# Performance work log

Hardware: AMD Instinct MI355X
Metric: run time of the kernel (lower is better)

## Reference

```python
import jax, jax.numpy as jnp
import numpy as np

B = 2048   # number of sessions
L = 128    # items per session (uniform sessions)
IDCG_FLOOR = 1e-5


def _pairwise_diff(t):
    # t: [L] -> [L, L] with m[i, j] = t[i] - t[j]
    return t[:, None] - t[None, :]


def _position_discounts(t):
    # rank of each element under descending sort, then 1/log2(rank+2)
    ranks = jnp.argsort(jnp.argsort(-t))
    return 1.0 / jnp.log2(ranks.astype(jnp.float32) + 2.0)


def _per_session(pred, label):
    # defaults: use_exp_gain=True, use_ndcg_as_loss=True, use_idcg_normalization=True
    gain = jnp.exp2(label).astype(jnp.float32)
    pred_disc = _position_discounts(pred)
    label_disc = _position_discounts(label)
    idcg = jnp.maximum(gain @ label_disc, IDCG_FLOOR)
    dcg = gain @ pred_disc
    session_weight = idcg  # use_idcg_normalization=True
    sign = jnp.sign(_pairwise_diff(label))
    pd_lxp = sign * _pairwise_diff(pred)
    lambda_mat = jnp.abs(_pairwise_diff(pred_disc) * _pairwise_diff(gain))
    loss = (idcg - dcg) / session_weight  # use_ndcg_as_loss=True
    grad_loss = jnp.sum(-lambda_mat * sign * jax.nn.sigmoid(-pd_lxp), axis=1) / session_weight
    return loss, grad_loss


def setup_inputs() -> dict:
    key = jax.random.key(0)
    k1, k2 = jax.random.split(key)
    logit = jax.random.normal(k1, (B * L,), dtype=jnp.float32)
    label = jax.random.randint(k2, (B * L,), 0, 5).astype(jnp.float32)
    return {"logit": logit, "label": label}


def reference(logit, label):
    # sessions are uniform length L, grouped contiguously -> reshape to [B, L]
    loss, grad_loss = jax.vmap(_per_session)(logit.reshape(B, L), label.reshape(B, L))
    return loss, grad_loss.reshape(-1)
```

## Files before the change

kernel.cpp:

```cpp
#include <hip/hip_runtime.h>
#include <math.h>

#define NSESS 2048
#define L 128
#define IDCG_FLOOR 1e-5f
#define LOG2E 1.44269504088896340736f

__device__ __forceinline__ float rl_f(float x, int j) {
    return __uint_as_float((unsigned)__builtin_amdgcn_readlane((int)__float_as_uint(x), j));
}
__device__ __forceinline__ unsigned rl_u(unsigned x, int j) {
    return (unsigned)__builtin_amdgcn_readlane((int)x, j);
}
__device__ __forceinline__ float fast_exp2(float x) {
    float r;
    asm("v_exp_f32 %0, %1" : "=v"(r) : "v"(x));
    return r;
}

__global__ __launch_bounds__(64) void lambdarank_ndcg_kernel(
    const float* __restrict__ logit,
    const float* __restrict__ label,
    float* __restrict__ out_loss,
    float* __restrict__ out_grad)
{
    const int b    = blockIdx.x;
    const int lane = threadIdx.x;
    const int base = b * L;

    const float p0  = logit[base + lane];
    const float p1  = logit[base + 64 + lane];
    const float lb0 = label[base + lane];
    const float lb1 = label[base + 64 + lane];
    const int   il0 = (int)lb0;
    const int   il1 = (int)lb1;
    const float g0  = (float)(1 << il0);
    const float g1  = (float)(1 << il1);

    const unsigned bb0  = __float_as_uint(p0);
    const unsigned bb1  = __float_as_uint(p1);
    const unsigned asc0 = (bb0 & 0x80000000u) ? ~bb0 : (bb0 | 0x80000000u);
    const unsigned asc1 = (bb1 & 0x80000000u) ? ~bb1 : (bb1 | 0x80000000u);
    const unsigned long long K0 =
        (((unsigned long long)(~asc0)) << 7) | (unsigned)lane;
    const unsigned long long K1 =
        (((unsigned long long)(~asc1)) << 7) | (unsigned)(lane + 64);

    int rp0 = 0, rp1 = 0;
    #pragma unroll 8
    for (int j = 0; j < 64; ++j) {
        const unsigned lo = rl_u((unsigned)K0, j);
        const unsigned hi = rl_u((unsigned)(K0 >> 32), j);
        const unsigned long long Kj = (((unsigned long long)hi) << 32) | lo;
        rp0 += (Kj < K0);
        rp1 += (Kj < K1);
    }
    #pragma unroll 8
    for (int j = 0; j < 64; ++j) {
        const unsigned lo = rl_u((unsigned)K1, j);
        const unsigned hi = rl_u((unsigned)(K1 >> 32), j);
        const unsigned long long Kj = (((unsigned long long)hi) << 32) | lo;
        rp0 += (Kj < K0);
        rp1 += (Kj < K1);
    }

    const unsigned long long lane_lt = (1ull << lane) - 1ull;
    int rl0 = 0, rl1 = 0;
    {
        int sumG = 0;
        #pragma unroll
        for (int v = 4; v >= 0; --v) {
            const unsigned long long m0 = __ballot(il0 == v);
            const unsigned long long m1 = __ballot(il1 == v);
            if (il0 == v) rl0 = sumG + __popcll(m0 & lane_lt);
            if (il1 == v) rl1 = sumG + __popcll(m0) + __popcll(m1 & lane_lt);
            sumG += __popcll(m0) + __popcll(m1);
        }
    }

    const float pd0 = __builtin_amdgcn_rcpf(log2f((float)(rp0 + 2)));
    const float pd1 = __builtin_amdgcn_rcpf(log2f((float)(rp1 + 2)));
    const float ld0 = __builtin_amdgcn_rcpf(log2f((float)(rl0 + 2)));
    const float ld1 = __builtin_amdgcn_rcpf(log2f((float)(rl1 + 2)));

    float dcg  = g0 * pd0 + g1 * pd1;
    float idcg = g0 * ld0 + g1 * ld1;
    #pragma unroll
    for (int off = 32; off > 0; off >>= 1) {
        dcg  += __shfl_xor(dcg,  off, 64);
        idcg += __shfl_xor(idcg, off, 64);
    }
    const float IDCG     = fmaxf(idcg, IDCG_FLOOR);
    const float inv_idcg = __builtin_amdgcn_rcpf(IDCG);

    const float ps0 = p0 * LOG2E;
    const float ps1 = p1 * LOG2E;
    float acc0 = 0.0f, acc1 = 0.0f;

    #pragma unroll 4
    for (int j = 0; j < 64; ++j) {
        const float pj = rl_f(ps0, j);
        const float gj = rl_f(g0,  j);
        const float dj = rl_f(pd0, j);
        {
            const float e  = fast_exp2(ps0 - pj);
            const float sg = __builtin_amdgcn_rcpf(1.0f + e);
            const float t  = (pd0 - dj) * (g0 - gj);
            const float nm = ((g0 < gj) ? 1.0f : 0.0f) - sg;
            acc0 += fabsf(t) * nm;
        }
        {
            const float e  = fast_exp2(ps1 - pj);
            const float sg = __builtin_amdgcn_rcpf(1.0f + e);
            const float t  = (pd1 - dj) * (g1 - gj);
            const float nm = ((g1 < gj) ? 1.0f : 0.0f) - sg;
            acc1 += fabsf(t) * nm;
        }
    }
    #pragma unroll 4
    for (int j = 0; j < 64; ++j) {
        const float pj = rl_f(ps1, j);
        const float gj = rl_f(g1,  j);
        const float dj = rl_f(pd1, j);
        {
            const float e  = fast_exp2(ps0 - pj);
            const float sg = __builtin_amdgcn_rcpf(1.0f + e);
            const float t  = (pd0 - dj) * (g0 - gj);
            const float nm = ((g0 < gj) ? 1.0f : 0.0f) - sg;
            acc0 += fabsf(t) * nm;
        }
        {
            const float e  = fast_exp2(ps1 - pj);
            const float sg = __builtin_amdgcn_rcpf(1.0f + e);
            const float t  = (pd1 - dj) * (g1 - gj);
            const float nm = ((g1 < gj) ? 1.0f : 0.0f) - sg;
            acc1 += fabsf(t) * nm;
        }
    }

    out_grad[base + lane]      = acc0 * inv_idcg;
    out_grad[base + 64 + lane] = acc1 * inv_idcg;
    if (lane == 0) out_loss[b] = (IDCG - dcg) * inv_idcg;
}

extern "C" void kernel_launch(void* const* d_in, const int* in_sizes, int n_in,
                              void* d_out, int out_size, void* d_ws, size_t ws_size,
                              hipStream_t stream) {
    const float* logit = (const float*)d_in[0];
    const float* label = (const float*)d_in[1];
    float* out      = (float*)d_out;
    float* out_loss = out;
    float* out_grad = out + NSESS;

    lambdarank_ndcg_kernel<<<NSESS, 64, 0, stream>>>(logit, label, out_loss, out_grad);
}
```

Measured before the change: 75.33 us.

## Factor sigmoid exponent into per-element exp products and vectorize loads

The per-pair exp2(pi - pj) is replaced by the product exp2(pi)*exp2(-pj), with both factors precomputed once per element. This removes one transcendental from the inner O(L^2) loop and leaves one multiply-add and one reciprocal per pair. Each lane now owns two adjacent elements, so loads and stores become float2, and the tie-break indices and label-rank prefix counts are adjusted to the interleaved order. Log and reciprocal use raw hardware instructions, and the unroll goes from 4 to 8. The product form can overflow to inf or underflow for large logit gaps, which changes precision at the extremes.

After: 72.51 us. -3.7%, faster.

```diff
diff --git a/kernel.cpp b/kernel.cpp
--- a/kernel.cpp
+++ b/kernel.cpp
@@ -12,11 +12,9 @@
 __device__ __forceinline__ unsigned rl_u(unsigned x, int j) {
     return (unsigned)__builtin_amdgcn_readlane((int)x, j);
 }
-__device__ __forceinline__ float fast_exp2(float x) {
-    float r;
-    asm("v_exp_f32 %0, %1" : "=v"(r) : "v"(x));
-    return r;
-}
+__device__ __forceinline__ float fexp2(float x){ float r; asm("v_exp_f32 %0, %1":"=v"(r):"v"(x)); return r; }
+__device__ __forceinline__ float flog2(float x){ float r; asm("v_log_f32 %0, %1":"=v"(r):"v"(x)); return r; }
+__device__ __forceinline__ float frcp (float x){ float r; asm("v_rcp_f32 %0, %1":"=v"(r):"v"(x)); return r; }
 
 __global__ __launch_bounds__(64) void lambdarank_ndcg_kernel(
     const float* __restrict__ logit,
@@ -28,10 +26,10 @@
     const int lane = threadIdx.x;
     const int base = b * L;
 
-    const float p0  = logit[base + lane];
-    const float p1  = logit[base + 64 + lane];
-    const float lb0 = label[base + lane];
-    const float lb1 = label[base + 64 + lane];
+    const float2 pv = ((const float2*)(logit + base))[lane];
+    const float2 lv = ((const float2*)(label + base))[lane];
+    const float p0  = pv.x,  p1  = pv.y;
+    const float lb0 = lv.x,  lb1 = lv.y;
     const int   il0 = (int)lb0;
     const int   il1 = (int)lb1;
     const float g0  = (float)(1 << il0);
@@ -42,9 +40,9 @@
     const unsigned asc0 = (bb0 & 0x80000000u) ? ~bb0 : (bb0 | 0x80000000u);
     const unsigned asc1 = (bb1 & 0x80000000u) ? ~bb1 : (bb1 | 0x80000000u);
     const unsigned long long K0 =
-        (((unsigned long long)(~asc0)) << 7) | (unsigned)lane;
+        (((unsigned long long)(~asc0)) << 7) | (unsigned)(2 * lane);
     const unsigned long long K1 =
-        (((unsigned long long)(~asc1)) << 7) | (unsigned)(lane + 64);
+        (((unsigned long long)(~asc1)) << 7) | (unsigned)(2 * lane + 1);
 
     int rp0 = 0, rp1 = 0;
     #pragma unroll 8
@@ -65,6 +63,7 @@
     }
 
     const unsigned long long lane_lt = (1ull << lane) - 1ull;
+    const unsigned long long lane_le = lane_lt | (1ull << lane);
     int rl0 = 0, rl1 = 0;
     {
         int sumG = 0;
@@ -72,16 +71,16 @@
         for (int v = 4; v >= 0; --v) {
             const unsigned long long m0 = __ballot(il0 == v);
             const unsigned long long m1 = __ballot(il1 == v);
-            if (il0 == v) rl0 = sumG + __popcll(m0 & lane_lt);
-            if (il1 == v) rl1 = sumG + __popcll(m0) + __popcll(m1 & lane_lt);
+            if (il0 == v) rl0 = sumG + __popcll(m0 & lane_lt) + __popcll(m1 & lane_lt);
+            if (il1 == v) rl1 = sumG + __popcll(m0 & lane_le) + __popcll(m1 & lane_lt);
             sumG += __popcll(m0) + __popcll(m1);
         }
     }
 
-    const float pd0 = __builtin_amdgcn_rcpf(log2f((float)(rp0 + 2)));
-    const float pd1 = __builtin_amdgcn_rcpf(log2f((float)(rp1 + 2)));
-    const float ld0 = __builtin_amdgcn_rcpf(log2f((float)(rl0 + 2)));
-    const float ld1 = __builtin_amdgcn_rcpf(log2f((float)(rl1 + 2)));
+    const float pd0 = frcp(flog2((float)(rp0 + 2)));
+    const float pd1 = frcp(flog2((float)(rp1 + 2)));
+    const float ld0 = frcp(flog2((float)(rl0 + 2)));
+    const float ld1 = frcp(flog2((float)(rl1 + 2)));
 
     float dcg  = g0 * pd0 + g1 * pd1;
     float idcg = g0 * ld0 + g1 * ld1;
@@ -91,55 +90,47 @@
         idcg += __shfl_xor(idcg, off, 64);
     }
     const float IDCG     = fmaxf(idcg, IDCG_FLOOR);
-    const float inv_idcg = __builtin_amdgcn_rcpf(IDCG);
+    const float inv_idcg = frcp(IDCG);
 
-    const float ps0 = p0 * LOG2E;
-    const float ps1 = p1 * LOG2E;
+    const float ps0   = p0 * LOG2E;
+    const float ps1   = p1 * LOG2E;
+    const float E0    = fexp2(ps0);
+    const float E1    = fexp2(ps1);
+    const float Einv0 = fexp2(-ps0);
+    const float Einv1 = fexp2(-ps1);
+
     float acc0 = 0.0f, acc1 = 0.0f;
 
-    #pragma unroll 4
+    #pragma unroll 8
     for (int j = 0; j < 64; ++j) {
-        const float pj = rl_f(ps0, j);
-        const float gj = rl_f(g0,  j);
-        const float dj = rl_f(pd0, j);
-        {
-            const float e  = fast_exp2(ps0 - pj);
-            const float sg = __builtin_amdgcn_rcpf(1.0f + e);
-            const float t  = (pd0 - dj) * (g0 - gj);
-            const float nm = ((g0 < gj) ? 1.0f : 0.0f) - sg;
-            acc0 += fabsf(t) * nm;
-        }
-        {
-            const float e  = fast_exp2(ps1 - pj);
-            const float sg = __builtin_amdgcn_rcpf(1.0f + e);
-            const float t  = (pd1 - dj) * (g1 - gj);
-            const float nm = ((g1 < gj) ? 1.0f : 0.0f) - sg;
-            acc1 += fabsf(t) * nm;
-        }
+        const float EJ = rl_f(Einv0, j);
+        const float gj = rl_f(g0,   j);
+        const float dj = rl_f(pd0,  j);
+        const float sg0 = frcp(1.0f + E0 * EJ);
+        const float sg1 = frcp(1.0f + E1 * EJ);
+        const float t0  = (pd0 - dj) * (g0 - gj);
+        const float t1  = (pd1 - dj) * (g1 - gj);
+        const float nm0 = ((g0 < gj) ? 1.0f : 0.0f) - sg0;
+        const float nm1 = ((g1 < gj) ? 1.0f : 0.0f) - sg1;
+        acc0 = fmaf(fabsf(t0), nm0, acc0);
+        acc1 = fmaf(fabsf(t1), nm1, acc1);
     }
-    #pragma unroll 4
+    #pragma unroll 8
     for (int j = 0; j < 64; ++j) {
-        const float pj = rl_f(ps1, j);
-        const float gj = rl_f(g1,  j);
-        const float dj = rl_f(pd1, j);
-        {
-            const float e  = fast_exp2(ps0 - pj);
-            const float sg = __builtin_amdgcn_rcpf(1.0f + e);
-            const float t  = (pd0 - dj) * (g0 - gj);
-            const float nm = ((g0 < gj) ? 1.0f : 0.0f) - sg;
-            acc0 += fabsf(t) * nm;
-        }
-        {
-            const float e  = fast_exp2(ps1 - pj);
-            const float sg = __builtin_amdgcn_rcpf(1.0f + e);
-            const float t  = (pd1 - dj) * (g1 - gj);
-            const float nm = ((g1 < gj) ? 1.0f : 0.0f) - sg;
-            acc1 += fabsf(t) * nm;
-        }
+        const float EJ = rl_f(Einv1, j);
+        const float gj = rl_f(g1,   j);
+        const float dj = rl_f(pd1,  j);
+        const float sg0 = frcp(1.0f + E0 * EJ);
+        const float sg1 = frcp(1.0f + E1 * EJ);
+        const float t0  = (pd0 - dj) * (g0 - gj);
+        const float t1  = (pd1 - dj) * (g1 - gj);
+        const float nm0 = ((g0 < gj) ? 1.0f : 0.0f) - sg0;
+        const float nm1 = ((g1 < gj) ? 1.0f : 0.0f) - sg1;
+        acc0 = fmaf(fabsf(t0), nm0, acc0);
+        acc1 = fmaf(fabsf(t1), nm1, acc1);
     }
 
-    out_grad[base + lane]      = acc0 * inv_idcg;
-    out_grad[base + 64 + lane] = acc1 * inv_idcg;
+    ((float2*)(out_grad + base))[lane] = make_float2(acc0 * inv_idcg, acc1 * inv_idcg);
     if (lane == 0) out_loss[b] = (IDCG - dcg) * inv_idcg;
 }
 
```
